# Optimization experiments

Measured on AMD Instinct MI355X. Metric: run time of the kernel, lower is better.

Reference implementation:

```python
import jax, jax.numpy as jnp
import numpy as np

IMG_SIZE = 416.0
CLASS_NUM = 80
NUM_ANCH = 3
MAX_GT = 64  # fixed padding for per-image valid GT boxes (original uses a variable-size python loop)


def _bce_logits(x, t):
    # BCEWithLogits, elementwise: softplus(x) - x*t  (numerically stable)
    return jax.nn.softplus(x) - x * t


def _make_noobj_mask(pred_boxes, targets):
    # pred_boxes: [B,G,G,3,4] in pixel units; targets: [B,G,G,3,85]
    B, G = pred_boxes.shape[0], pred_boxes.shape[1]
    N = G * G * NUM_ANCH
    conf = targets[..., 4].reshape(B, N)
    boxes = targets[..., 0:4].reshape(B, N, 4)
    # gather up to MAX_GT ground-truth boxes per image (conf>0 are the valid ones)
    top_conf, idx = jax.lax.top_k(conf, MAX_GT)            # [B,M]
    gt = jnp.take_along_axis(boxes, idx[..., None], axis=1)  # [B,M,4]
    valid = top_conf > 0.0                                   # [B,M]

    p = pred_boxes.reshape(B, N, 4)
    pxy = p[:, :, None, 0:2]   # [B,N,1,2]
    pwh = p[:, :, None, 2:4]
    gxy = gt[:, None, :, 0:2]  # [B,1,M,2]
    gwh = gt[:, None, :, 2:4]

    imin = jnp.maximum(pxy - pwh / 2, gxy - gwh / 2)
    imax = jnp.minimum(pxy + pwh / 2, gxy + gwh / 2)
    iwh = jnp.maximum(imax - imin, 0.0)
    inter = iwh[..., 0] * iwh[..., 1]                        # [B,N,M]
    area_p = pwh[..., 0] * pwh[..., 1]
    area_g = gwh[..., 0] * gwh[..., 1]
    iou = inter / (area_p + area_g - inter + 1e-9)
    iou = jnp.where(valid[:, None, :], iou, 0.0)
    best_iou = jnp.max(iou, axis=-1)                         # [B,N]
    noobj = (best_iou < 0.6).astype(pred_boxes.dtype)
    return noobj.reshape(B, G, G, NUM_ANCH)


def reference(preds, targets, anchors):
    B, G = preds.shape[0], preds.shape[1]
    ratio = IMG_SIZE / G
    p = preds.reshape(B, G, G, NUM_ANCH, 5 + CLASS_NUM)
    box_xy_raw, box_wh_raw, conf_logit, cls_logit = jnp.split(p, [2, 4, 5], axis=-1)

    # grid offsets: offset[i,j] = (j, i)
    gx, gy = jnp.meshgrid(jnp.arange(G, dtype=preds.dtype), jnp.arange(G, dtype=preds.dtype))
    offset = jnp.stack([gx, gy], axis=-1).reshape(G, G, 1, 2)

    sig_xy = jax.nn.sigmoid(box_xy_raw)
    box_xy = (sig_xy + offset) * ratio                 # pixel units
    box_wh = jnp.exp(box_wh_raw) * anchors             # (anchors/ratio)*ratio = anchors
    pred_boxes = jnp.concatenate([box_xy, box_wh], axis=-1)

    preds_xy = box_xy / ratio - offset                 # == sig_xy
    true_xy = targets[..., 0:2] / ratio - offset
    true_wh = targets[..., 2:4] / anchors
    preds_wh = box_wh / anchors
    true_wh = jnp.where(true_wh == 0.0, 1.0, true_wh)
    preds_wh = jnp.where(preds_wh == 0.0, 1.0, preds_wh)
    true_wh = jnp.log(jnp.clip(true_wh, 1e-9, 1e9))
    preds_wh = jnp.log(jnp.clip(preds_wh, 1e-9, 1e9))

    obj = (targets[..., 4] > 0.0).astype(preds.dtype)  # [B,G,G,3]
    obj_e = obj[..., None]
    scale = 2.0 - targets[..., 2:3] / IMG_SIZE * targets[..., 3:4] / IMG_SIZE  # [B,G,G,3,1]

    txty_loss = jnp.sum(obj_e * (preds_xy - true_xy) ** 2 * scale) / B
    twth_loss = jnp.sum(obj_e * (preds_wh - true_wh) ** 2 * scale) / B

    noobj = _make_noobj_mask(pred_boxes, targets)      # [B,G,G,3]
    noobj_conf_mask = (1.0 - obj) * noobj
    conf_t = targets[..., 4:5]
    noobj_conf_loss = jnp.sum(noobj_conf_mask[..., None] * _bce_logits(conf_logit, conf_t)) / B
    obj_conf_loss = jnp.sum(obj_e * _bce_logits(conf_logit, conf_t)) / B
    class_loss = jnp.sum(obj_e * _bce_logits(cls_logit, targets[..., 5:])) / B

    total_loss = txty_loss + twth_loss + noobj_conf_loss + obj_conf_loss + class_loss
    return (txty_loss, twth_loss, noobj_conf_loss, obj_conf_loss, class_loss, total_loss)


def setup_inputs() -> dict:
    key = jax.random.key(0)
    ks = jax.random.split(key, 5)
    B, G, A, C = 32, 52, NUM_ANCH, CLASS_NUM
    N = G * G * A
    M_OBJ = 40  # GT boxes per image (< MAX_GT)
    preds = jax.random.normal(ks[0], (B, G, G, A * (5 + C)), jnp.float32) * 0.5
    idx = jax.random.randint(ks[1], (B, M_OBJ), 0, N)
    xy = jax.random.uniform(ks[2], (B, M_OBJ, 2), jnp.float32, 0.0, IMG_SIZE)
    wh = jax.random.uniform(ks[3], (B, M_OBJ, 2), jnp.float32, 16.0, 128.0)
    cid = jax.random.randint(ks[4], (B, M_OBJ), 0, C)
    onehot = jax.nn.one_hot(cid, C, dtype=jnp.float32)
    vals = jnp.concatenate([xy, wh, jnp.ones((B, M_OBJ, 1), jnp.float32), onehot], axis=-1)
    t = jnp.zeros((B, N, 5 + C), jnp.float32)
    t = t.at[jnp.arange(B)[:, None], idx].set(vals)
    targets = t.reshape(B, G, G, A, 5 + C)
    anchors = jnp.array([[10.0, 13.0], [16.0, 30.0], [33.0, 23.0]], jnp.float32)
    return {"preds": preds, "targets": targets, "anchors": anchors}
```

## Files before the change

kernel.cpp:

```cpp
#include <hip/hip_runtime.h>
#include <math.h>

#define GSZ 52
#define NA 3
#define NCLS 80
#define CH 85
#define NCA (GSZ*GSZ*NA)
#define MAXGT 64
#define MCHUNK 32
#define CLSBLK 16

__device__ __forceinline__ float softplus_fast(float x) {
    return fmaxf(x, 0.0f) + __logf(1.0f + __expf(-fabsf(x)));
}

__global__ void k_init(int* cnt, int B) {
    if (threadIdx.x < B) cnt[threadIdx.x] = 0;
}

__device__ __forceinline__ void emit_gt(const float* __restrict__ tg, int glob,
                                        int* cnt, float4* __restrict__ gtbox,
                                        int2* __restrict__ gtinfo) {
    const float* r = tg + (size_t)glob * CH;
    int b    = glob / NCA;
    int nloc = glob - b * NCA;
    int cid = 0;
#pragma unroll 16
    for (int c = 0; c < NCLS; c++) if (r[5 + c] > 0.5f) cid = c;
    int pos = atomicAdd(cnt + b, 1);
    if (pos < MAXGT) {
        gtbox[b * MAXGT + pos]  = make_float4(r[0], r[1], r[2], r[3]);
        gtinfo[b * MAXGT + pos] = make_int2(nloc, cid);
    }
}

__global__ void k_scan(const float* __restrict__ tg, const float* __restrict__ pr,
                       const float* __restrict__ anchors, int nrec, int* cnt,
                       float4* __restrict__ gtbox, int2* __restrict__ gtinfo,
                       float4* __restrict__ boxdec, float* __restrict__ confdec) {
    int rec = blockIdx.x * 256 + threadIdx.x;
    if (rec >= nrec) return;

    float conf_t = tg[(size_t)rec * CH + 4];
    const float* r = pr + (size_t)rec * CH;
    float r0 = r[0], r1 = r[1], r2 = r[2], r3 = r[3], pc = r[4];

    int b    = rec / NCA;
    int n    = rec - b * NCA;
    int a    = n % NA;
    int cell = n / NA;
    int gi = cell / GSZ, gj = cell % GSZ;
    float aw = anchors[2 * a], ah = anchors[2 * a + 1];

    float sx = __builtin_amdgcn_rcpf(1.0f + __expf(-r0));
    float sy = __builtin_amdgcn_rcpf(1.0f + __expf(-r1));
    float bx = (sx + (float)gj) * 8.0f;
    float by = (sy + (float)gi) * 8.0f;
    float bw = __expf(r2) * aw;
    float bh = __expf(r3) * ah;

    boxdec[rec]  = make_float4(bx, by, bw, bh);
    confdec[rec] = pc;

    if (conf_t > 0.0f) emit_gt(tg, rec, cnt, gtbox, gtinfo);
}

__global__ void k_nc(const float* __restrict__ pr,
                     const float* __restrict__ anchors,
                     const int* __restrict__ cnt,
                     const float4* __restrict__ gtbox,
                     const int2* __restrict__ gtinfo,
                     const float4* __restrict__ boxdec,
                     const float* __restrict__ confdec,
                     float* __restrict__ partial,
                     float4* __restrict__ cls4) {
    int b   = blockIdx.y;
    int tid = threadIdx.x;

    if (blockIdx.x < MCHUNK) {
        __shared__ float4 sbox[MAXGT];
        __shared__ int    sidx[MAXGT];
        __shared__ float  swsum[4];

        int n = blockIdx.x * 256 + tid;
        int m = min(cnt[b], MAXGT);
        if (tid < m) {
            sbox[tid] = gtbox[b * MAXGT + tid];
            sidx[tid] = gtinfo[b * MAXGT + tid].x;
        }
        __syncthreads();

        float v = 0.0f;
        if (n < NCA) {
            size_t rec = (size_t)b * NCA + n;
            float4 pb = boxdec[rec];
            float  pc = confdec[rec];
            float px0 = pb.x - pb.z * 0.5f, px1 = pb.x + pb.z * 0.5f;
            float py0 = pb.y - pb.w * 0.5f, py1 = pb.y + pb.w * 0.5f;
            float areap = pb.z * pb.w;

            float best = 0.0f;
            bool isobj = false;
            for (int k = 0; k < m; k++) {
                float4 g = sbox[k];
                isobj |= (sidx[k] == n);
                float ix = fminf(px1, g.x + g.z * 0.5f) - fmaxf(px0, g.x - g.z * 0.5f);
                float iy = fminf(py1, g.y + g.w * 0.5f) - fmaxf(py0, g.y - g.w * 0.5f);
                float inter = fmaxf(ix, 0.0f) * fmaxf(iy, 0.0f);
                float u = areap + g.z * g.w - inter + 1e-9f;
                best = fmaxf(best, inter * __builtin_amdgcn_rcpf(u));
            }
            if (!isobj && best < 0.6f) v = softplus_fast(pc);
        }

        int lane = tid & 63;
        int wv   = tid >> 6;
        for (int off = 32; off > 0; off >>= 1) v += __shfl_down(v, off);
        if (lane == 0) swsum[wv] = v;
        __syncthreads();
        if (tid == 0) {
            partial[b * MCHUNK + blockIdx.x] = swsum[0] + swsum[1] + swsum[2] + swsum[3];
        }
    } else {
        int wv   = tid >> 6;
        int lane = tid & 63;
        int slot = b * MAXGT + (blockIdx.x - MCHUNK) * 4 + wv;
        int k    = slot & (MAXGT - 1);

        float4 resv = make_float4(0.f, 0.f, 0.f, 0.f);
        int m = min(cnt[b], MAXGT);
        if (k < m) {
            float4 g  = gtbox[slot];
            int2 info = gtinfo[slot];
            int n = info.x, cid = info.y;
            size_t rec = (size_t)b * NCA + n;
            const float* cl = pr + rec * CH + 5;

            float x0 = cl[lane];
            float cls = softplus_fast(x0) - (lane == cid ? x0 : 0.0f);
            if (lane < NCLS - 64) {
                float x1 = cl[64 + lane];
                cls += softplus_fast(x1) - ((64 + lane) == cid ? x1 : 0.0f);
            }
            for (int off = 32; off > 0; off >>= 1) cls += __shfl_down(cls, off);

            if (lane == 0) {
                float4 pb = boxdec[rec];
                float  pc = confdec[rec];
                int a    = n % NA;
                int cell = n / NA;
                int gi = cell / GSZ, gj = cell % GSZ;
                float aw = anchors[2 * a], ah = anchors[2 * a + 1];

                float scale = 2.0f - (g.z * (1.0f / 416.0f)) * (g.w * (1.0f / 416.0f));
                float dx = (pb.x * 0.125f - (float)gj) - (g.x * 0.125f - (float)gj);
                float dy = (pb.y * 0.125f - (float)gi) - (g.y * 0.125f - (float)gi);
                float txty = (dx * dx + dy * dy) * scale;

                float rw = __builtin_amdgcn_rcpf(aw), rh = __builtin_amdgcn_rcpf(ah);
                float pwr = fminf(fmaxf(pb.z * rw, 1e-9f), 1e9f);
                float phr = fminf(fmaxf(pb.w * rh, 1e-9f), 1e9f);
                float twr = fminf(fmaxf(g.z  * rw, 1e-9f), 1e9f);
                float thr = fminf(fmaxf(g.w  * rh, 1e-9f), 1e9f);
                float dw = __logf(pwr) - __logf(twr);
                float dh = __logf(phr) - __logf(thr);
                float twth = (dw * dw + dh * dh) * scale;

                float obj = softplus_fast(pc) - pc;
                resv = make_float4(txty, twth, obj, cls);
            }
        }
        if (lane == 0) cls4[slot] = resv;
    }
}

__global__ void k_final(const float* __restrict__ partial, int np,
                        const float4* __restrict__ cls4, int ns,
                        int B, float* __restrict__ out) {
    __shared__ double sred[4 * 5];
    int tid = threadIdx.x;
    double acc[5] = {0, 0, 0, 0, 0};
    for (int i = tid; i < np; i += 256) acc[2] += (double)partial[i];
    for (int i = tid; i < ns; i += 256) {
        float4 v = cls4[i];
        acc[0] += (double)v.x; acc[1] += (double)v.y;
        acc[3] += (double)v.z; acc[4] += (double)v.w;
    }
    int lane = tid & 63;
    int wv   = tid >> 6;
#pragma unroll
    for (int i = 0; i < 5; i++) {
        double v = acc[i];
        for (int off = 32; off > 0; off >>= 1) v += __shfl_down(v, off);
        if (lane == 0) sred[wv * 5 + i] = v;
    }
    __syncthreads();
    if (tid == 0) {
        double tot = 0.0;
#pragma unroll
        for (int i = 0; i < 5; i++) {
            double r = (sred[i] + sred[5 + i] + sred[10 + i] + sred[15 + i]) / (double)B;
            out[i] = (float)r;
            tot += r;
        }
        out[5] = (float)tot;
    }
}

extern "C" void kernel_launch(void* const* d_in, const int* in_sizes, int n_in,
                              void* d_out, int out_size, void* d_ws, size_t ws_size,
                              hipStream_t stream) {
    const float* preds   = (const float*)d_in[0];
    const float* targets = (const float*)d_in[1];
    const float* anchors = (const float*)d_in[2];
    float* out = (float*)d_out;

    int B = in_sizes[0] / (NCA * CH);
    int nrec = B * NCA;
    int scan_blocks = (nrec + 255) / 256;
    int np = MCHUNK * B;
    int ns = B * MAXGT;

    char* ws = (char*)d_ws;
    size_t off = 0;
    int*    cnt     = (int*)(ws + off);      off += 128;
    float4* gtbox   = (float4*)(ws + off);   off += (size_t)ns * sizeof(float4);
    int2*   gtinfo  = (int2*)(ws + off);     off += (size_t)ns * sizeof(int2);
    float*  partial = (float*)(ws + off);    off += (size_t)np * sizeof(float);
    off = (off + 15) & ~(size_t)15;
    float4* boxdec  = (float4*)(ws + off);   off += (size_t)nrec * sizeof(float4);
    float*  confdec = (float*)(ws + off);    off += (size_t)nrec * sizeof(float);
    off = (off + 15) & ~(size_t)15;
    float4* cls4    = (float4*)(ws + off);   off += (size_t)ns * sizeof(float4);

    k_init<<<1, 64, 0, stream>>>(cnt, B);
    k_scan<<<scan_blocks, 256, 0, stream>>>(targets, preds, anchors, nrec, cnt,
                                            gtbox, gtinfo, boxdec, confdec);
    dim3 grid(MCHUNK + CLSBLK, B);
    k_nc<<<grid, 256, 0, stream>>>(preds, anchors, cnt, gtbox, gtinfo,
                                   boxdec, confdec, partial, cls4);
    k_final<<<1, 256, 0, stream>>>(partial, np, cls4, ns, B, out);
}
```

Before: 196.6 us.

## Fuse all stages into one cooperative persistent kernel with grid syncs

```diff
diff --git a/kernel.cpp b/kernel.cpp
--- a/kernel.cpp
+++ b/kernel.cpp
@@ -1,5 +1,8 @@
 #include <hip/hip_runtime.h>
+#include <hip/hip_cooperative_groups.h>
 #include <math.h>
+
+namespace cg = cooperative_groups;
 
 #define GSZ 52
 #define NA 3
@@ -8,14 +11,10 @@
 #define NCA (GSZ*GSZ*NA)
 #define MAXGT 64
 #define MCHUNK 32
-#define CLSBLK 16
+#define CLSU 16
 
 __device__ __forceinline__ float softplus_fast(float x) {
     return fmaxf(x, 0.0f) + __logf(1.0f + __expf(-fabsf(x)));
-}
-
-__global__ void k_init(int* cnt, int B) {
-    if (threadIdx.x < B) cnt[threadIdx.x] = 0;
 }
 
 __device__ __forceinline__ void emit_gt(const float* __restrict__ tg, int glob,
@@ -34,176 +33,191 @@
     }
 }
 
-__global__ void k_scan(const float* __restrict__ tg, const float* __restrict__ pr,
-                       const float* __restrict__ anchors, int nrec, int* cnt,
-                       float4* __restrict__ gtbox, int2* __restrict__ gtinfo,
-                       float4* __restrict__ boxdec, float* __restrict__ confdec) {
-    int rec = blockIdx.x * 256 + threadIdx.x;
-    if (rec >= nrec) return;
-
-    float conf_t = tg[(size_t)rec * CH + 4];
-    const float* r = pr + (size_t)rec * CH;
-    float r0 = r[0], r1 = r[1], r2 = r[2], r3 = r[3], pc = r[4];
-
-    int b    = rec / NCA;
-    int n    = rec - b * NCA;
-    int a    = n % NA;
-    int cell = n / NA;
-    int gi = cell / GSZ, gj = cell % GSZ;
-    float aw = anchors[2 * a], ah = anchors[2 * a + 1];
-
-    float sx = __builtin_amdgcn_rcpf(1.0f + __expf(-r0));
-    float sy = __builtin_amdgcn_rcpf(1.0f + __expf(-r1));
-    float bx = (sx + (float)gj) * 8.0f;
-    float by = (sy + (float)gi) * 8.0f;
-    float bw = __expf(r2) * aw;
-    float bh = __expf(r3) * ah;
-
-    boxdec[rec]  = make_float4(bx, by, bw, bh);
-    confdec[rec] = pc;
-
-    if (conf_t > 0.0f) emit_gt(tg, rec, cnt, gtbox, gtinfo);
-}
-
-__global__ void k_nc(const float* __restrict__ pr,
-                     const float* __restrict__ anchors,
-                     const int* __restrict__ cnt,
-                     const float4* __restrict__ gtbox,
-                     const int2* __restrict__ gtinfo,
-                     const float4* __restrict__ boxdec,
-                     const float* __restrict__ confdec,
-                     float* __restrict__ partial,
-                     float4* __restrict__ cls4) {
-    int b   = blockIdx.y;
-    int tid = threadIdx.x;
-
-    if (blockIdx.x < MCHUNK) {
-        __shared__ float4 sbox[MAXGT];
-        __shared__ int    sidx[MAXGT];
-        __shared__ float  swsum[4];
-
-        int n = blockIdx.x * 256 + tid;
-        int m = min(cnt[b], MAXGT);
-        if (tid < m) {
-            sbox[tid] = gtbox[b * MAXGT + tid];
-            sidx[tid] = gtinfo[b * MAXGT + tid].x;
-        }
-        __syncthreads();
-
-        float v = 0.0f;
-        if (n < NCA) {
-            size_t rec = (size_t)b * NCA + n;
-            float4 pb = boxdec[rec];
-            float  pc = confdec[rec];
-            float px0 = pb.x - pb.z * 0.5f, px1 = pb.x + pb.z * 0.5f;
-            float py0 = pb.y - pb.w * 0.5f, py1 = pb.y + pb.w * 0.5f;
-            float areap = pb.z * pb.w;
-
-            float best = 0.0f;
-            bool isobj = false;
-            for (int k = 0; k < m; k++) {
-                float4 g = sbox[k];
-                isobj |= (sidx[k] == n);
-                float ix = fminf(px1, g.x + g.z * 0.5f) - fmaxf(px0, g.x - g.z * 0.5f);
-                float iy = fminf(py1, g.y + g.w * 0.5f) - fmaxf(py0, g.y - g.w * 0.5f);
-                float inter = fmaxf(ix, 0.0f) * fmaxf(iy, 0.0f);
-                float u = areap + g.z * g.w - inter + 1e-9f;
-                best = fmaxf(best, inter * __builtin_amdgcn_rcpf(u));
-            }
-            if (!isobj && best < 0.6f) v = softplus_fast(pc);
-        }
-
-        int lane = tid & 63;
-        int wv   = tid >> 6;
-        for (int off = 32; off > 0; off >>= 1) v += __shfl_down(v, off);
-        if (lane == 0) swsum[wv] = v;
-        __syncthreads();
-        if (tid == 0) {
-            partial[b * MCHUNK + blockIdx.x] = swsum[0] + swsum[1] + swsum[2] + swsum[3];
-        }
-    } else {
-        int wv   = tid >> 6;
-        int lane = tid & 63;
-        int slot = b * MAXGT + (blockIdx.x - MCHUNK) * 4 + wv;
-        int k    = slot & (MAXGT - 1);
-
-        float4 resv = make_float4(0.f, 0.f, 0.f, 0.f);
-        int m = min(cnt[b], MAXGT);
-        if (k < m) {
-            float4 g  = gtbox[slot];
-            int2 info = gtinfo[slot];
-            int n = info.x, cid = info.y;
-            size_t rec = (size_t)b * NCA + n;
-            const float* cl = pr + rec * CH + 5;
-
-            float x0 = cl[lane];
-            float cls = softplus_fast(x0) - (lane == cid ? x0 : 0.0f);
-            if (lane < NCLS - 64) {
-                float x1 = cl[64 + lane];
-                cls += softplus_fast(x1) - ((64 + lane) == cid ? x1 : 0.0f);
-            }
-            for (int off = 32; off > 0; off >>= 1) cls += __shfl_down(cls, off);
-
-            if (lane == 0) {
-                float4 pb = boxdec[rec];
-                float  pc = confdec[rec];
+__global__ __launch_bounds__(256) void k_all(
+    const float* __restrict__ tg, const float* __restrict__ pr,
+    const float* __restrict__ anchors, int B, int* cnt,
+    float4* __restrict__ gtbox, int2* __restrict__ gtinfo,
+    float4* __restrict__ boxdec, float* __restrict__ confdec,
+    float* __restrict__ partial, float4* __restrict__ cls4,
+    float* __restrict__ out)
+{
+    cg::grid_group grid = cg::this_grid();
+    __shared__ float4 sbox[MAXGT];
+    __shared__ int    sidx[MAXGT];
+    __shared__ float  swsum[4];
+    __shared__ double sred[4 * 5];
+
+    const int tid  = threadIdx.x;
+    const int bid  = blockIdx.x;
+    const int G    = gridDim.x;
+    const int gtid = bid * 256 + tid;
+    const int nrec = B * NCA;
+
+    if (bid == 0 && tid < B) cnt[tid] = 0;
+    grid.sync();
+
+    {
+        const int stride = G * 256;
+        const int ntask  = 2 * nrec;
+        for (int t = gtid; t < ntask; t += stride) {
+            int rec = t >> 1;
+            const float* rp = pr + (size_t)rec * CH;
+            if (t & 1) {
+                float pc     = rp[4];
+                float conf_t = tg[(size_t)rec * CH + 4];
+                confdec[rec] = pc;
+                if (conf_t > 0.0f) emit_gt(tg, rec, cnt, gtbox, gtinfo);
+            } else {
+                float r0 = rp[0], r1 = rp[1], r2 = rp[2], r3 = rp[3];
+                int b    = rec / NCA;
+                int n    = rec - b * NCA;
                 int a    = n % NA;
                 int cell = n / NA;
                 int gi = cell / GSZ, gj = cell % GSZ;
                 float aw = anchors[2 * a], ah = anchors[2 * a + 1];
-
-                float scale = 2.0f - (g.z * (1.0f / 416.0f)) * (g.w * (1.0f / 416.0f));
-                float dx = (pb.x * 0.125f - (float)gj) - (g.x * 0.125f - (float)gj);
-                float dy = (pb.y * 0.125f - (float)gi) - (g.y * 0.125f - (float)gi);
-                float txty = (dx * dx + dy * dy) * scale;
-
-                float rw = __builtin_amdgcn_rcpf(aw), rh = __builtin_amdgcn_rcpf(ah);
-                float pwr = fminf(fmaxf(pb.z * rw, 1e-9f), 1e9f);
-                float phr = fminf(fmaxf(pb.w * rh, 1e-9f), 1e9f);
-                float twr = fminf(fmaxf(g.z  * rw, 1e-9f), 1e9f);
-                float thr = fminf(fmaxf(g.w  * rh, 1e-9f), 1e9f);
-                float dw = __logf(pwr) - __logf(twr);
-                float dh = __logf(phr) - __logf(thr);
-                float twth = (dw * dw + dh * dh) * scale;
-
-                float obj = softplus_fast(pc) - pc;
-                resv = make_float4(txty, twth, obj, cls);
+                float sx = __builtin_amdgcn_rcpf(1.0f + __expf(-r0));
+                float sy = __builtin_amdgcn_rcpf(1.0f + __expf(-r1));
+                float bx = (sx + (float)gj) * 8.0f;
+                float by = (sy + (float)gi) * 8.0f;
+                float bw = __expf(r2) * aw;
+                float bh = __expf(r3) * ah;
+                boxdec[rec] = make_float4(bx, by, bw, bh);
             }
         }
-        if (lane == 0) cls4[slot] = resv;
-    }
-}
-
-__global__ void k_final(const float* __restrict__ partial, int np,
-                        const float4* __restrict__ cls4, int ns,
-                        int B, float* __restrict__ out) {
-    __shared__ double sred[4 * 5];
-    int tid = threadIdx.x;
-    double acc[5] = {0, 0, 0, 0, 0};
-    for (int i = tid; i < np; i += 256) acc[2] += (double)partial[i];
-    for (int i = tid; i < ns; i += 256) {
-        float4 v = cls4[i];
-        acc[0] += (double)v.x; acc[1] += (double)v.y;
-        acc[3] += (double)v.z; acc[4] += (double)v.w;
-    }
-    int lane = tid & 63;
-    int wv   = tid >> 6;
-#pragma unroll
-    for (int i = 0; i < 5; i++) {
-        double v = acc[i];
-        for (int off = 32; off > 0; off >>= 1) v += __shfl_down(v, off);
-        if (lane == 0) sred[wv * 5 + i] = v;
-    }
-    __syncthreads();
-    if (tid == 0) {
-        double tot = 0.0;
+    }
+    grid.sync();
+
+    {
+        const int nu    = B * MCHUNK;
+        const int units = nu + B * CLSU;
+        for (int u = bid; u < units; u += G) {
+            if (u < nu) {
+                int b     = u >> 5;
+                int chunk = u & (MCHUNK - 1);
+                int n = chunk * 256 + tid;
+                int m = min(cnt[b], MAXGT);
+                if (tid < m) {
+                    sbox[tid] = gtbox[b * MAXGT + tid];
+                    sidx[tid] = gtinfo[b * MAXGT + tid].x;
+                }
+                __syncthreads();
+
+                float v = 0.0f;
+                if (n < NCA) {
+                    size_t rec = (size_t)b * NCA + n;
+                    float4 pb = boxdec[rec];
+                    float  pc = confdec[rec];
+                    float px0 = pb.x - pb.z * 0.5f, px1 = pb.x + pb.z * 0.5f;
+                    float py0 = pb.y - pb.w * 0.5f, py1 = pb.y + pb.w * 0.5f;
+                    float areap = pb.z * pb.w;
+
+                    float best = 0.0f;
+                    bool isobj = false;
+                    for (int k = 0; k < m; k++) {
+                        float4 g = sbox[k];
+                        isobj |= (sidx[k] == n);
+                        float ix = fminf(px1, g.x + g.z * 0.5f) - fmaxf(px0, g.x - g.z * 0.5f);
+                        float iy = fminf(py1, g.y + g.w * 0.5f) - fmaxf(py0, g.y - g.w * 0.5f);
+                        float inter = fmaxf(ix, 0.0f) * fmaxf(iy, 0.0f);
+                        float uu = areap + g.z * g.w - inter + 1e-9f;
+                        best = fmaxf(best, inter * __builtin_amdgcn_rcpf(uu));
+                    }
+                    if (!isobj && best < 0.6f) v = softplus_fast(pc);
+                }
+
+                int lane = tid & 63;
+                int wv   = tid >> 6;
+                for (int off = 32; off > 0; off >>= 1) v += __shfl_down(v, off);
+                if (lane == 0) swsum[wv] = v;
+                __syncthreads();
+                if (tid == 0)
+                    partial[u] = swsum[0] + swsum[1] + swsum[2] + swsum[3];
+            } else {
+                int wv   = tid >> 6;
+                int lane = tid & 63;
+                int slot = (u - nu) * 4 + wv;
+                int b    = slot >> 6;
+                int k    = slot & (MAXGT - 1);
+
+                float4 resv = make_float4(0.f, 0.f, 0.f, 0.f);
+                int m = min(cnt[b], MAXGT);
+                if (k < m) {
+                    float4 g  = gtbox[slot];
+                    int2 info = gtinfo[slot];
+                    int n = info.x, cid = info.y;
+                    size_t rec = (size_t)b * NCA + n;
+                    const float* cl = pr + rec * CH + 5;
+
+                    float x0 = cl[lane];
+                    float cls = softplus_fast(x0) - (lane == cid ? x0 : 0.0f);
+                    if (lane < NCLS - 64) {
+                        float x1 = cl[64 + lane];
+                        cls += softplus_fast(x1) - ((64 + lane) == cid ? x1 : 0.0f);
+                    }
+                    for (int off = 32; off > 0; off >>= 1) cls += __shfl_down(cls, off);
+
+                    if (lane == 0) {
+                        float4 pb = boxdec[rec];
+                        float  pc = confdec[rec];
+                        int a    = n % NA;
+                        int cell = n / NA;
+                        int gi = cell / GSZ, gj = cell % GSZ;
+                        float aw = anchors[2 * a], ah = anchors[2 * a + 1];
+
+                        float scale = 2.0f - (g.z * (1.0f / 416.0f)) * (g.w * (1.0f / 416.0f));
+                        float dx = (pb.x * 0.125f - (float)gj) - (g.x * 0.125f - (float)gj);
+                        float dy = (pb.y * 0.125f - (float)gi) - (g.y * 0.125f - (float)gi);
+                        float txty = (dx * dx + dy * dy) * scale;
+
+                        float rw = __builtin_amdgcn_rcpf(aw), rh = __builtin_amdgcn_rcpf(ah);
+                        float pwr = fminf(fmaxf(pb.z * rw, 1e-9f), 1e9f);
+                        float phr = fminf(fmaxf(pb.w * rh, 1e-9f), 1e9f);
+                        float twr = fminf(fmaxf(g.z  * rw, 1e-9f), 1e9f);
+                        float thr = fminf(fmaxf(g.w  * rh, 1e-9f), 1e9f);
+                        float dw = __logf(pwr) - __logf(twr);
+                        float dh = __logf(phr) - __logf(thr);
+                        float twth = (dw * dw + dh * dh) * scale;
+
+                        float obj = softplus_fast(pc) - pc;
+                        resv = make_float4(txty, twth, obj, cls);
+                    }
+                }
+                if (lane == 0) cls4[slot] = resv;
+            }
+            __syncthreads();
+        }
+    }
+    grid.sync();
+
+    if (bid == 0) {
+        const int np = B * MCHUNK;
+        const int ns = B * MAXGT;
+        double acc[5] = {0, 0, 0, 0, 0};
+        for (int i = tid; i < np; i += 256) acc[2] += (double)partial[i];
+        for (int i = tid; i < ns; i += 256) {
+            float4 v = cls4[i];
+            acc[0] += (double)v.x; acc[1] += (double)v.y;
+            acc[3] += (double)v.z; acc[4] += (double)v.w;
+        }
+        int lane = tid & 63;
+        int wv   = tid >> 6;
 #pragma unroll
         for (int i = 0; i < 5; i++) {
-            double r = (sred[i] + sred[5 + i] + sred[10 + i] + sred[15 + i]) / (double)B;
-            out[i] = (float)r;
-            tot += r;
-        }
-        out[5] = (float)tot;
+            double v = acc[i];
+            for (int off = 32; off > 0; off >>= 1) v += __shfl_down(v, off);
+            if (lane == 0) sred[wv * 5 + i] = v;
+        }
+        __syncthreads();
+        if (tid == 0) {
+            double tot = 0.0;
+#pragma unroll
+            for (int i = 0; i < 5; i++) {
+                double r = (sred[i] + sred[5 + i] + sred[10 + i] + sred[15 + i]) / (double)B;
+                out[i] = (float)r;
+                tot += r;
+            }
+            out[5] = (float)tot;
+        }
     }
 }
 
@@ -217,7 +231,6 @@
 
     int B = in_sizes[0] / (NCA * CH);
     int nrec = B * NCA;
-    int scan_blocks = (nrec + 255) / 256;
     int np = MCHUNK * B;
     int ns = B * MAXGT;
 
@@ -233,11 +246,22 @@
     off = (off + 15) & ~(size_t)15;
     float4* cls4    = (float4*)(ws + off);   off += (size_t)ns * sizeof(float4);
 
-    k_init<<<1, 64, 0, stream>>>(cnt, B);
-    k_scan<<<scan_blocks, 256, 0, stream>>>(targets, preds, anchors, nrec, cnt,
-                                            gtbox, gtinfo, boxdec, confdec);
-    dim3 grid(MCHUNK + CLSBLK, B);
-    k_nc<<<grid, 256, 0, stream>>>(preds, anchors, cnt, gtbox, gtinfo,
-                                   boxdec, confdec, partial, cls4);
-    k_final<<<1, 256, 0, stream>>>(partial, np, cls4, ns, B, out);
-}
+    static int G = 0;
+    if (G == 0) {
+        hipDeviceProp_t prop;
+        hipGetDeviceProperties(&prop, 0);
+        int perCU = 0;
+        hipOccupancyMaxActiveBlocksPerMultiprocessor(&perCU, (const void*)k_all, 256, 0);
+        if (perCU < 1) perCU = 1;
+        G = prop.multiProcessorCount * perCU;
+        if (G < 256) G = 256;
+        if (G > 4096) G = 4096;
+    }
+
+    void* args[] = {(void*)&targets, (void*)&preds, (void*)&anchors, (void*)&B,
+                    (void*)&cnt, (void*)&gtbox, (void*)&gtinfo,
+                    (void*)&boxdec, (void*)&confdec,
+                    (void*)&partial, (void*)&cls4, (void*)&out};
+    hipLaunchCooperativeKernel((const void*)k_all, dim3(G), dim3(256),
+                               args, 0, stream);
+}
```

After: 612.8 us. 212% more time.
